# Kernel tuning notes

Hardware: AMD Instinct MI355X
Metric: run time of the kernel (lower is better)

Reference implementation:

```python
import jax, jax.numpy as jnp
import numpy as np

PAD_TOKEN = 0

def setup_inputs() -> dict:
    key = jax.random.key(0)
    ks = jax.random.split(key, 6)
    B, S, E, W, V = 16, 2048, 128, 128, 7
    x = jax.random.randint(ks[0], (B, S), 0, V, dtype=jnp.int64)
    emb_table = jax.random.normal(ks[1], (V, E), dtype=jnp.float32)
    fc_w = jax.random.normal(ks[2], (E, W * E), dtype=jnp.float32) * 0.02
    fc_b = jax.random.normal(ks[3], (E,), dtype=jnp.float32) * 0.02
    out_w = jax.random.normal(ks[4], (1, E), dtype=jnp.float32) * 0.02
    out_b = jax.random.normal(ks[5], (1,), dtype=jnp.float32) * 0.02
    return {"x": x, "emb_table": emb_table, "fc_w": fc_w, "fc_b": fc_b,
            "out_w": out_w, "out_b": out_b}

def reference(x, emb_table, fc_w, fc_b, out_w, out_b):
    B, S = x.shape
    V, E = emb_table.shape
    Eo, WE = fc_w.shape
    W = WE // E
    # embedding lookup: [B, S, E]
    ex = emb_table[x]
    # causal left pad by W-1 along seq -> [B, S+W-1, E]
    padded = jnp.pad(ex, ((0, 0), (W - 1, 0), (0, 0)))
    # torch unfold gives windows[b,s,e,k] = padded[b, s+k, e], flattened index e*W + k.
    # Equivalent implicit conv: kernel[k, e, o] = fc_w[o, e*W + k]  (WIO layout)
    kernel = jnp.transpose(fc_w.reshape(Eo, E, W), (2, 1, 0))
    conv = jax.lax.conv_general_dilated(
        padded, kernel, window_strides=(1,), padding='VALID',
        dimension_numbers=('NWC', 'WIO', 'NWC'))  # [B, S, Eo]
    h = conv + fc_b
    # output_layer: Linear(E -> 1), then squeeze -> [B, S]
    logits = jnp.einsum('bse,oe->bso', h, out_w)[..., 0] + out_b[0]
    # return_last_seq=True: gather at last non-pad count index
    last_idx = jnp.sum(x != PAD_TOKEN, axis=-1) - 1  # [B]
    out = logits[jnp.arange(B), last_idx].reshape(-1, 1)
    return out
```

## Files before the change

kernel.cpp:

```cpp
#include <hip/hip_runtime.h>

#define BB 16
#define SS 2048
#define EE 128
#define WW 128
#define VV 7
#define WE (WW * EE)

__global__ __launch_bounds__(256) void fused(const int* __restrict__ x,
                                             const float* __restrict__ emb,
                                             const float* __restrict__ fc_w,
                                             const float* __restrict__ fc_b,
                                             const float* __restrict__ out_w,
                                             const float* __restrict__ out_b,
                                             float* __restrict__ out) {
    __shared__ float red[16][64];
    __shared__ float v[64];
    __shared__ float embS[8];
    __shared__ int lastS[BB];
    __shared__ float bred[2];
    __shared__ float s_bias;

    const int c = blockIdx.x;
    const int t = threadIdx.x;
    const int lane = t & 63;
    const int w = t >> 6;
    const int e = c >> 1;
    const int k0 = (c & 1) * 64;

    const int oo = lane >> 4;
    const int kq = lane & 15;
    const float* fbase = fc_w + (size_t)e * WW + k0 + kq * 4;
    float4 f[8];
    float ow[8];
#pragma unroll
    for (int it = 0; it < 8; ++it) {
        const int o = w * 32 + it * 4 + oo;
        f[it] = *reinterpret_cast<const float4*>(fbase + (size_t)o * WE);
        ow[it] = out_w[o];
    }

    if (t >= 64 && t < 72) {
        const int tok = t - 64;
        embS[tok] = (tok < VV) ? emb[tok * EE + e] : 0.f;
    }

    if (c == 0) {
        float p = (t < EE) ? out_w[t] * fc_b[t] : 0.f;
#pragma unroll
        for (int off = 32; off; off >>= 1) p += __shfl_down(p, off, 64);
        if (lane == 0 && w < 2) bred[w] = p;
    }

    const int bt = t >> 4;
    const int ch = t & 15;
    const int4* xp = reinterpret_cast<const int4*>(x + bt * SS + ch * 128);
    int cnt = 0;
#pragma unroll
    for (int i = 0; i < 32; ++i) {
        const int4 q = xp[i];
        cnt += (q.x != 0) + (q.y != 0) + (q.z != 0) + (q.w != 0);
    }
#pragma unroll
    for (int off = 8; off; off >>= 1) cnt += __shfl_down(cnt, off, 16);
    if (ch == 0) lastS[bt] = cnt - 1;

    float4 acc = make_float4(0.f, 0.f, 0.f, 0.f);
#pragma unroll
    for (int it = 0; it < 8; ++it) {
        acc.x += ow[it] * f[it].x;
        acc.y += ow[it] * f[it].y;
        acc.z += ow[it] * f[it].z;
        acc.w += ow[it] * f[it].w;
    }
    *reinterpret_cast<float4*>(&red[w * 4 + oo][kq * 4]) = acc;
    __syncthreads();
    if (t < 64) {
        float s = 0.f;
#pragma unroll
        for (int g = 0; g < 16; ++g) s += red[g][t];
        v[t] = s;
    }
    if (c == 0 && t == 0) s_bias = bred[0] + bred[1] + out_b[0];
    __syncthreads();

    const int b = t >> 4;
    const int kg = t & 15;
    const int last = lastS[b];
    const int* xb = x + b * SS;
    float val = 0.f;
#pragma unroll
    for (int q2 = 0; q2 < 4; ++q2) {
        const int k = k0 + kg * 4 + q2;
        const int j = last - (WW - 1) + k;
        const int tok = (j >= 0) ? xb[j] : VV;
        val += v[kg * 4 + q2] * embS[tok];
    }
#pragma unroll
    for (int off = 8; off; off >>= 1) val += __shfl_down(val, off, 16);
    if (kg == 0) {
        if (c == 0) val += s_bias;
        atomicAdd(&out[b], val);
    }
}

extern "C" void kernel_launch(void* const* d_in, const int* in_sizes, int n_in,
                              void* d_out, int out_size, void* d_ws, size_t ws_size,
                              hipStream_t stream) {
    const int* x = (const int*)d_in[0];
    const float* emb = (const float*)d_in[1];
    const float* fc_w = (const float*)d_in[2];
    const float* fc_b = (const float*)d_in[3];
    const float* out_w = (const float*)d_in[4];
    const float* out_b = (const float*)d_in[5];
    float* out = (float*)d_out;

    fused<<<256, 256, 0, stream>>>(x, emb, fc_w, fc_b, out_w, out_b, out);
}
```

Baseline: 87.19 us.

## Replace output atomics with last-block reduction and coalesce token count loads

Each block now writes its per-batch partial sums to a workspace buffer instead of atomically adding into the output. A global counter picks out the last block to finish, and that block sums all partials and writes the output directly. The intent is to avoid the separate output zeroing or memset and the contended atomics on 16 addresses. The token-count loop is also re-indexed so adjacent threads read adjacent int4 values. The counter relies on the workspace being poisoned to 0xAAAAAAAA on first use, then counting modulo 256 across calls, which is a fragile assumption about the harness.

```diff
diff --git a/kernel.cpp b/kernel.cpp
--- a/kernel.cpp
+++ b/kernel.cpp
@@ -6,6 +6,7 @@
 #define WW 128
 #define VV 7
 #define WE (WW * EE)
+#define POISON_I ((int)0xAAAAAAAA)
 
 __global__ __launch_bounds__(256) void fused(const int* __restrict__ x,
                                              const float* __restrict__ emb,
@@ -13,6 +14,8 @@
                                              const float* __restrict__ fc_b,
                                              const float* __restrict__ out_w,
                                              const float* __restrict__ out_b,
+                                             int* __restrict__ done,
+                                             float* __restrict__ part,
                                              float* __restrict__ out) {
     __shared__ float red[16][64];
     __shared__ float v[64];
@@ -20,6 +23,8 @@
     __shared__ int lastS[BB];
     __shared__ float bred[2];
     __shared__ float s_bias;
+    __shared__ int s_isLast;
+    __shared__ float mat[16][17];
 
     const int c = blockIdx.x;
     const int t = threadIdx.x;
@@ -45,7 +50,7 @@
         embS[tok] = (tok < VV) ? emb[tok * EE + e] : 0.f;
     }
 
-    if (c == 0) {
+    {
         float p = (t < EE) ? out_w[t] * fc_b[t] : 0.f;
 #pragma unroll
         for (int off = 32; off; off >>= 1) p += __shfl_down(p, off, 64);
@@ -54,11 +59,11 @@
 
     const int bt = t >> 4;
     const int ch = t & 15;
-    const int4* xp = reinterpret_cast<const int4*>(x + bt * SS + ch * 128);
+    const int4* xq = reinterpret_cast<const int4*>(x);
     int cnt = 0;
 #pragma unroll
     for (int i = 0; i < 32; ++i) {
-        const int4 q = xp[i];
+        const int4 q = xq[bt * 512 + i * 16 + ch];
         cnt += (q.x != 0) + (q.y != 0) + (q.z != 0) + (q.w != 0);
     }
 #pragma unroll
@@ -81,7 +86,7 @@
         for (int g = 0; g < 16; ++g) s += red[g][t];
         v[t] = s;
     }
-    if (c == 0 && t == 0) s_bias = bred[0] + bred[1] + out_b[0];
+    if (t == 0) s_bias = bred[0] + bred[1] + out_b[0];
     __syncthreads();
 
     const int b = t >> 4;
@@ -98,9 +103,32 @@
     }
 #pragma unroll
     for (int off = 8; off; off >>= 1) val += __shfl_down(val, off, 16);
-    if (kg == 0) {
-        if (c == 0) val += s_bias;
-        atomicAdd(&out[b], val);
+    if (kg == 0) atomicExch(&part[c * 16 + b], val);
+
+    __syncthreads();
+    if (t == 0) {
+        __threadfence();
+        atomicCAS(done, POISON_I, 0);
+        const int old = atomicAdd(done, 1);
+        s_isLast = ((old & 255) == 255);
+    }
+    __syncthreads();
+    if (!s_isLast) return;
+
+    __threadfence();
+    const int g = t >> 4;
+    const int b2 = t & 15;
+    float s = 0.f;
+#pragma unroll
+    for (int i = 0; i < 16; ++i)
+        s += part[(g * 16 + i) * 16 + b2];
+    mat[g][b2] = s;
+    __syncthreads();
+    if (t < BB) {
+        float tot = s_bias;
+#pragma unroll
+        for (int gg = 0; gg < 16; ++gg) tot += mat[gg][t];
+        out[t] = tot;
     }
 }
 
@@ -113,7 +141,9 @@
     const float* fc_b = (const float*)d_in[3];
     const float* out_w = (const float*)d_in[4];
     const float* out_b = (const float*)d_in[5];
+    int* done = (int*)d_ws;
+    float* part = (float*)((char*)d_ws + 64);
     float* out = (float*)d_out;
 
-    fused<<<256, 256, 0, stream>>>(x, emb, fc_w, fc_b, out_w, out_b, out);
+    fused<<<256, 256, 0, stream>>>(x, emb, fc_w, fc_b, out_w, out_b, done, part, out);
 }
```

New measurement: 82.85 us. 1.05x faster.

## Replace atomic output accumulation with partial buffer and second reduction kernel

Applied to the files above, without the earlier changes.

The fused kernel no longer atomically adds each block's partial sum into the output. It writes per-block partials to workspace, and a new single-block kernel sums them together with the bias term. The pad-count loads are also reordered so adjacent threads read adjacent int4 values, giving coalesced access. This removes the 4096 same-address atomics and the reliance on a pre-zeroed output, at the cost of a second kernel launch and a workspace round trip.

```diff
diff --git a/kernel.cpp b/kernel.cpp
--- a/kernel.cpp
+++ b/kernel.cpp
@@ -7,19 +7,15 @@
 #define VV 7
 #define WE (WW * EE)
 
-__global__ __launch_bounds__(256) void fused(const int* __restrict__ x,
-                                             const float* __restrict__ emb,
-                                             const float* __restrict__ fc_w,
-                                             const float* __restrict__ fc_b,
-                                             const float* __restrict__ out_w,
-                                             const float* __restrict__ out_b,
-                                             float* __restrict__ out) {
+__global__ __launch_bounds__(256) void k1_slice(const int* __restrict__ x,
+                                                const float* __restrict__ emb,
+                                                const float* __restrict__ fc_w,
+                                                const float* __restrict__ out_w,
+                                                float* __restrict__ part) {
     __shared__ float red[16][64];
     __shared__ float v[64];
     __shared__ float embS[8];
     __shared__ int lastS[BB];
-    __shared__ float bred[2];
-    __shared__ float s_bias;
 
     const int c = blockIdx.x;
     const int t = threadIdx.x;
@@ -45,20 +41,13 @@
         embS[tok] = (tok < VV) ? emb[tok * EE + e] : 0.f;
     }
 
-    if (c == 0) {
-        float p = (t < EE) ? out_w[t] * fc_b[t] : 0.f;
-#pragma unroll
-        for (int off = 32; off; off >>= 1) p += __shfl_down(p, off, 64);
-        if (lane == 0 && w < 2) bred[w] = p;
-    }
-
     const int bt = t >> 4;
     const int ch = t & 15;
-    const int4* xp = reinterpret_cast<const int4*>(x + bt * SS + ch * 128);
+    const int4* xq = reinterpret_cast<const int4*>(x);
     int cnt = 0;
 #pragma unroll
     for (int i = 0; i < 32; ++i) {
-        const int4 q = xp[i];
+        const int4 q = xq[bt * 512 + i * 16 + ch];
         cnt += (q.x != 0) + (q.y != 0) + (q.z != 0) + (q.w != 0);
     }
 #pragma unroll
@@ -81,7 +70,6 @@
         for (int g = 0; g < 16; ++g) s += red[g][t];
         v[t] = s;
     }
-    if (c == 0 && t == 0) s_bias = bred[0] + bred[1] + out_b[0];
     __syncthreads();
 
     const int b = t >> 4;
@@ -98,9 +86,39 @@
     }
 #pragma unroll
     for (int off = 8; off; off >>= 1) val += __shfl_down(val, off, 16);
-    if (kg == 0) {
-        if (c == 0) val += s_bias;
-        atomicAdd(&out[b], val);
+    if (kg == 0) part[c * 16 + b] = val;
+}
+
+__global__ __launch_bounds__(256) void k2_reduce(const float* __restrict__ part,
+                                                 const float* __restrict__ fc_b,
+                                                 const float* __restrict__ out_w,
+                                                 const float* __restrict__ out_b,
+                                                 float* __restrict__ out) {
+    __shared__ float mat[16][17];
+    __shared__ float bred[2];
+
+    const int t = threadIdx.x;
+    const int lane = t & 63;
+    const int w = t >> 6;
+
+    float p = (t < EE) ? out_w[t] * fc_b[t] : 0.f;
+#pragma unroll
+    for (int off = 32; off; off >>= 1) p += __shfl_down(p, off, 64);
+    if (lane == 0 && w < 2) bred[w] = p;
+
+    const int g = t >> 4;
+    const int b = t & 15;
+    float s = 0.f;
+#pragma unroll
+    for (int i = 0; i < 16; ++i)
+        s += part[(g * 16 + i) * 16 + b];
+    mat[g][b] = s;
+    __syncthreads();
+    if (t < BB) {
+        float tot = bred[0] + bred[1] + out_b[0];
+#pragma unroll
+        for (int gg = 0; gg < 16; ++gg) tot += mat[gg][t];
+        out[t] = tot;
     }
 }
 
@@ -113,7 +131,9 @@
     const float* fc_b = (const float*)d_in[3];
     const float* out_w = (const float*)d_in[4];
     const float* out_b = (const float*)d_in[5];
+    float* part = (float*)d_ws;
     float* out = (float*)d_out;
 
-    fused<<<256, 256, 0, stream>>>(x, emb, fc_w, fc_b, out_w, out_b, out);
+    k1_slice<<<256, 256, 0, stream>>>(x, emb, fc_w, out_w, part);
+    k2_reduce<<<1, 256, 0, stream>>>(part, fc_b, out_w, out_b, out);
 }
```

Result: faster. 73.72 us (-15.4%).
